# Kernel tuning notes

Hardware: AMD Instinct MI355X
Metric: run time of the kernel (lower is better)

## Reference

```python
import jax, jax.numpy as jnp
import numpy as np

B, D_IN, H, D_OUT, K = 8192, 2048, 2048, 1024, 4
LOGVAR_INIT = -5.0


def setup_inputs() -> dict:
    key = jax.random.key(0)
    ks = jax.random.split(key, 32)
    dims = [(D_IN, H), (H, H), (H, D_OUT)]
    inp = {"x": jax.random.normal(ks[0], (B, D_IN), dtype=jnp.float32)}
    i = 1
    for l, (din, dout) in enumerate(dims):
        inp[f"w_mu{l}"] = 0.1 * jax.random.normal(ks[i], (K, dout, din), dtype=jnp.float32); i += 1
        inp[f"b_mu{l}"] = 0.1 * jax.random.normal(ks[i], (K, dout), dtype=jnp.float32); i += 1
        inp[f"w_lv{l}"] = jnp.full((K,), LOGVAR_INIT, dtype=jnp.float32)
        inp[f"b_lv{l}"] = jnp.full((K,), LOGVAR_INIT, dtype=jnp.float32)
        inp[f"ml{l}"] = jnp.zeros((K,), dtype=jnp.float32)
        # reparameterization noise (randn_like in the torch code), one per component
        inp[f"w_n{l}"] = jax.random.normal(ks[i], (K, dout, din), dtype=jnp.float32); i += 1
        inp[f"b_n{l}"] = jax.random.normal(ks[i], (K, dout), dtype=jnp.float32); i += 1
    return inp


def _mixture_linear(x, w_mu, b_mu, w_lv, b_lv, ml, w_n, b_n):
    # n_components <= n_samples: all K components used, weighted by softmax(mix_logits)
    mix_w = jax.nn.softmax(ml)                               # [K]
    w = w_mu + jnp.exp(0.5 * w_lv)[:, None, None] * w_n      # [K, O, I]
    b = b_mu + jnp.exp(0.5 * b_lv)[:, None] * b_n            # [K, O]
    # sum_k mix_w[k] * (x @ w[k].T + b[k])
    out = jnp.einsum('bi,koi,k->bo', x, w, mix_w)
    out = out + jnp.einsum('k,ko->o', mix_w, b)
    return out


def reference(x,
              w_mu0, b_mu0, w_lv0, b_lv0, ml0, w_n0, b_n0,
              w_mu1, b_mu1, w_lv1, b_lv1, ml1, w_n1, b_n1,
              w_mu2, b_mu2, w_lv2, b_lv2, ml2, w_n2, b_n2):
    h = jax.nn.relu(_mixture_linear(x, w_mu0, b_mu0, w_lv0, b_lv0, ml0, w_n0, b_n0))
    h = jax.nn.relu(_mixture_linear(h, w_mu1, b_mu1, w_lv1, b_lv1, ml1, w_n1, b_n1))
    h = _mixture_linear(h, w_mu2, b_mu2, w_lv2, b_lv2, ml2, w_n2, b_n2)
    return jax.nn.softmax(h, axis=1)
```

## Files before the change

kernel.cpp:

```cpp
#include <hip/hip_runtime.h>
#include <hip/hip_fp16.h>

typedef _Float16 half8 __attribute__((ext_vector_type(8)));
typedef _Float16 half4 __attribute__((ext_vector_type(4)));
typedef float floatx16 __attribute__((ext_vector_type(16)));

#define GLDS16(g, l)                                                           \
  __builtin_amdgcn_global_load_lds(                                            \
      (const __attribute__((address_space(1))) void*)(g),                      \
      (__attribute__((address_space(3))) void*)(l), 16, 0, 0)

__device__ inline void mix_coeffs(const float* lv, const float* ml,
                                  float* cmu, float* cn) {
  float m0 = ml[0], m1 = ml[1], m2 = ml[2], m3 = ml[3];
  float mx = fmaxf(fmaxf(m0, m1), fmaxf(m2, m3));
  float e0 = __expf(m0 - mx), e1 = __expf(m1 - mx);
  float e2 = __expf(m2 - mx), e3 = __expf(m3 - mx);
  float inv = 1.0f / (e0 + e1 + e2 + e3);
  cmu[0] = e0 * inv; cmu[1] = e1 * inv; cmu[2] = e2 * inv; cmu[3] = e3 * inv;
  cn[0] = cmu[0] * __expf(0.5f * lv[0]);
  cn[1] = cmu[1] * __expf(0.5f * lv[1]);
  cn[2] = cmu[2] * __expf(0.5f * lv[2]);
  cn[3] = cmu[3] * __expf(0.5f * lv[3]);
}

__device__ inline void do_prep_w(const float* __restrict__ mu,
                                 const float* __restrict__ nz,
                                 const float* lv, const float* ml,
                                 _Float16* __restrict__ out, long count4,
                                 int bid) {
  float cmu[4], cn[4];
  mix_coeffs(lv, ml, cmu, cn);
  long i = (long)bid * 256 + threadIdx.x;
  const float4* m4 = (const float4*)mu;
  const float4* n4 = (const float4*)nz;
  float4 a0 = m4[0 * count4 + i];
  float4 a1 = m4[1 * count4 + i];
  float4 a2 = m4[2 * count4 + i];
  float4 a3 = m4[3 * count4 + i];
  float4 b0 = n4[0 * count4 + i];
  float4 b1 = n4[1 * count4 + i];
  float4 b2 = n4[2 * count4 + i];
  float4 b3 = n4[3 * count4 + i];
  float rx = cmu[0]*a0.x + cn[0]*b0.x + cmu[1]*a1.x + cn[1]*b1.x
           + cmu[2]*a2.x + cn[2]*b2.x + cmu[3]*a3.x + cn[3]*b3.x;
  float ry = cmu[0]*a0.y + cn[0]*b0.y + cmu[1]*a1.y + cn[1]*b1.y
           + cmu[2]*a2.y + cn[2]*b2.y + cmu[3]*a3.y + cn[3]*b3.y;
  float rz = cmu[0]*a0.z + cn[0]*b0.z + cmu[1]*a1.z + cn[1]*b1.z
           + cmu[2]*a2.z + cn[2]*b2.z + cmu[3]*a3.z + cn[3]*b3.z;
  float rw = cmu[0]*a0.w + cn[0]*b0.w + cmu[1]*a1.w + cn[1]*b1.w
           + cmu[2]*a2.w + cn[2]*b2.w + cmu[3]*a3.w + cn[3]*b3.w;
  half4 h = {(_Float16)rx, (_Float16)ry, (_Float16)rz, (_Float16)rw};
  *(half4*)(out + i * 4) = h;
}

__device__ inline void do_prep_b(const float* __restrict__ bmu,
                                 const float* __restrict__ bn,
                                 const float* lv, const float* ml,
                                 float* __restrict__ out, int O, int bid) {
  float cmu[4], cn[4];
  mix_coeffs(lv, ml, cmu, cn);
  int i = bid * 256 + threadIdx.x;
  if (i >= O) return;
  float r = 0.f;
#pragma unroll
  for (int k = 0; k < 4; ++k)
    r += cmu[k] * bmu[k * O + i] + cn[k] * bn[k * O + i];
  out[i] = r;
}

__device__ inline void do_cvt(const float* __restrict__ in,
                              _Float16* __restrict__ out, int bid) {
  long i = ((long)bid * 256 + threadIdx.x) * 4;
  float4 v = *(const float4*)(in + i);
  half4 h = {(_Float16)v.x, (_Float16)v.y, (_Float16)v.z, (_Float16)v.w};
  *(half4*)(out + i) = h;
}

struct PrepArgs {
  const float* x; _Float16* x16;
  const float* wmu0; const float* wn0; const float* wlv0; const float* ml0; _Float16* W0;
  const float* wmu1; const float* wn1; const float* wlv1; const float* ml1; _Float16* W1;
  const float* wmu2; const float* wn2; const float* wlv2; const float* ml2; _Float16* W2;
  const float* bmu0; const float* bn0; const float* blv0; float* b0;
  const float* bmu1; const float* bn1; const float* blv1; float* b1;
  const float* bmu2; const float* bn2; const float* blv2; float* b2;
};

__global__ __launch_bounds__(256) void prep_all(PrepArgs a) {
  for (int wb = blockIdx.x; wb < 26644; wb += 2048) {
    if (wb < 4096) {
      do_prep_w(a.wmu0, a.wn0, a.wlv0, a.ml0, a.W0, 1048576, wb);
    } else if (wb < 8192) {
      do_prep_w(a.wmu1, a.wn1, a.wlv1, a.ml1, a.W1, 1048576, wb - 4096);
    } else if (wb < 10240) {
      do_prep_w(a.wmu2, a.wn2, a.wlv2, a.ml2, a.W2, 524288, wb - 8192);
    } else if (wb < 26624) {
      do_cvt(a.x, a.x16, wb - 10240);
    } else if (wb < 26632) {
      do_prep_b(a.bmu0, a.bn0, a.blv0, a.ml0, a.b0, 2048, wb - 26624);
    } else if (wb < 26640) {
      do_prep_b(a.bmu1, a.bn1, a.blv1, a.ml1, a.b1, 2048, wb - 26632);
    } else {
      do_prep_b(a.bmu2, a.bn2, a.blv2, a.ml2, a.b2, 1024, wb - 26640);
    }
  }
}

template <bool RELU, bool OUT_HALF>
__global__ __launch_bounds__(256, 3) void gemm_nt(
    const _Float16* __restrict__ A, const _Float16* __restrict__ B,
    const float* __restrict__ bias, void* __restrict__ Cout,
    int M, int N, int K) {
  __shared__ _Float16 sA[128 * 64];
  __shared__ _Float16 sB[128 * 64];

  const int t = threadIdx.x;
  const int l = t & 63;
  const int w = t >> 6;
  const int wr = w >> 1;
  const int wc = w & 1;
  const long rowBlock = (long)blockIdx.y * 128;
  const long colBlock = (long)blockIdx.x * 128;

  floatx16 acc[2][2] = {};

  const _Float16* ga[4];
  const _Float16* gb[4];
#pragma unroll
  for (int j = 0; j < 4; ++j) {
    int p = j * 256 + t;
    int r = p >> 3, pos = p & 7;
    int gc = pos ^ (r & 7);
    ga[j] = A + (rowBlock + r) * (long)K + gc * 8;
    gb[j] = B + (colBlock + r) * (long)K + gc * 8;
  }
  char* stA = (char*)sA + w * 1024;
  char* stB = (char*)sB + w * 1024;

  const int rm = l & 31;
  const int kh = l >> 5;
  const int sw = rm & 7;

  for (int k0 = 0; k0 < K; k0 += 64) {
#pragma unroll
    for (int j = 0; j < 4; ++j) GLDS16(ga[j] + k0, stA + j * 4096);
#pragma unroll
    for (int j = 0; j < 4; ++j) GLDS16(gb[j] + k0, stB + j * 4096);
    __syncthreads();
#pragma unroll
    for (int s = 0; s < 4; ++s) {
      const int pos = (s * 2 + kh) ^ sw;
      half8 af[2], bf[2];
#pragma unroll
      for (int rt = 0; rt < 2; ++rt)
        af[rt] = *(const half8*)((const char*)sA +
                                 ((wr * 64 + rt * 32 + rm) * 128 + pos * 16));
#pragma unroll
      for (int ct = 0; ct < 2; ++ct)
        bf[ct] = *(const half8*)((const char*)sB +
                                 ((wc * 64 + ct * 32 + rm) * 128 + pos * 16));
#pragma unroll
      for (int rt = 0; rt < 2; ++rt)
#pragma unroll
        for (int ct = 0; ct < 2; ++ct)
          acc[rt][ct] = __builtin_amdgcn_mfma_f32_32x32x16_f16(
              af[rt], bf[ct], acc[rt][ct], 0, 0, 0);
    }
    __syncthreads();
  }

  const int cl = l & 31;
  const int rh = (l >> 5) * 4;
#pragma unroll
  for (int rt = 0; rt < 2; ++rt) {
#pragma unroll
    for (int ct = 0; ct < 2; ++ct) {
      const long colg = colBlock + wc * 64 + ct * 32 + cl;
      const float bv = bias[colg];
#pragma unroll
      for (int reg = 0; reg < 16; ++reg) {
        const int rowin = (reg & 3) + 8 * (reg >> 2) + rh;
        const long rowg = rowBlock + wr * 64 + rt * 32 + rowin;
        float v = acc[rt][ct][reg] + bv;
        if (RELU) v = fmaxf(v, 0.0f);
        if (OUT_HALF)
          ((_Float16*)Cout)[rowg * N + colg] = (_Float16)v;
        else
          ((float*)Cout)[rowg * N + colg] = v;
      }
    }
  }
}

__global__ __launch_bounds__(256) void softmax_rows(float* __restrict__ io) {
  const int N = 1024;
  float* p = io + (long)blockIdx.x * N;
  int t = threadIdx.x;
  int w = t >> 6;
  float4 v = ((const float4*)p)[t];
  float m = fmaxf(fmaxf(v.x, v.y), fmaxf(v.z, v.w));
#pragma unroll
  for (int off = 32; off > 0; off >>= 1) m = fmaxf(m, __shfl_xor(m, off));
  __shared__ float red[8];
  if ((t & 63) == 0) red[w] = m;
  __syncthreads();
  m = fmaxf(fmaxf(red[0], red[1]), fmaxf(red[2], red[3]));
  float4 e;
  e.x = __expf(v.x - m); e.y = __expf(v.y - m);
  e.z = __expf(v.z - m); e.w = __expf(v.w - m);
  float s = e.x + e.y + e.z + e.w;
#pragma unroll
  for (int off = 32; off > 0; off >>= 1) s += __shfl_xor(s, off);
  if ((t & 63) == 0) red[4 + w] = s;
  __syncthreads();
  s = red[4] + red[5] + red[6] + red[7];
  float inv = 1.0f / s;
  float4 o = {e.x * inv, e.y * inv, e.z * inv, e.w * inv};
  ((float4*)p)[t] = o;
}

extern "C" void kernel_launch(void* const* d_in, const int* in_sizes, int n_in,
                              void* d_out, int out_size, void* d_ws,
                              size_t ws_size, hipStream_t stream) {
  char* ws = (char*)d_ws;
  _Float16* x16 = (_Float16*)(ws);
  _Float16* h0  = (_Float16*)(ws + 33554432);
  _Float16* W0  = (_Float16*)(ws + 67108864);
  _Float16* W1  = (_Float16*)(ws + 75497472);
  _Float16* W2  = (_Float16*)(ws + 83886080);
  float* b0 = (float*)(ws + 88080384);
  float* b1 = (float*)(ws + 88088576);
  float* b2 = (float*)(ws + 88096768);

  PrepArgs a;
  a.x = (const float*)d_in[0]; a.x16 = x16;
  a.wmu0 = (const float*)d_in[1];  a.bmu0 = (const float*)d_in[2];
  a.wlv0 = (const float*)d_in[3];  a.blv0 = (const float*)d_in[4];
  a.ml0  = (const float*)d_in[5];
  a.wn0  = (const float*)d_in[6];  a.bn0  = (const float*)d_in[7];
  a.wmu1 = (const float*)d_in[8];  a.bmu1 = (const float*)d_in[9];
  a.wlv1 = (const float*)d_in[10]; a.blv1 = (const float*)d_in[11];
  a.ml1  = (const float*)d_in[12];
  a.wn1  = (const float*)d_in[13]; a.bn1  = (const float*)d_in[14];
  a.wmu2 = (const float*)d_in[15]; a.bmu2 = (const float*)d_in[16];
  a.wlv2 = (const float*)d_in[17]; a.blv2 = (const float*)d_in[18];
  a.ml2  = (const float*)d_in[19];
  a.wn2  = (const float*)d_in[20]; a.bn2  = (const float*)d_in[21];
  a.W0 = W0; a.W1 = W1; a.W2 = W2; a.b0 = b0; a.b1 = b1; a.b2 = b2;

  prep_all<<<2048, 256, 0, stream>>>(a);

  gemm_nt<true, true><<<dim3(16, 64), 256, 0, stream>>>(
      x16, W0, b0, h0, 8192, 2048, 2048);
  gemm_nt<true, true><<<dim3(16, 64), 256, 0, stream>>>(
      h0, W1, b1, x16, 8192, 2048, 2048);
  gemm_nt<false, false><<<dim3(8, 64), 256, 0, stream>>>(
      x16, W2, b2, d_out, 8192, 1024, 2048);
  softmax_rows<<<8192, 256, 0, stream>>>((float*)d_out);
}
```

Before: 617.8 us.

## Double-buffer GEMM LDS tiles, swizzle block order, and widen prep work per thread

The GEMM now uses two LDS buffers per operand and issues the global-to-LDS loads for the next K-slice before computing the current one, removing one barrier per iteration and overlapping load latency with MFMA work. Work-group ids are remapped with an XCD-style swizzle onto a 1D grid to improve L2 locality. Occupancy is lowered to 2 blocks per CU because LDS use doubles. The prep kernel also processes four float4 chunks per thread with a flat grid instead of a grid-stride loop.

```diff
diff --git a/kernel.cpp b/kernel.cpp
--- a/kernel.cpp
+++ b/kernel.cpp
@@ -24,34 +24,51 @@
   cn[3] = cmu[3] * __expf(0.5f * lv[3]);
 }
 
-__device__ inline void do_prep_w(const float* __restrict__ mu,
-                                 const float* __restrict__ nz,
-                                 const float* lv, const float* ml,
-                                 _Float16* __restrict__ out, long count4,
-                                 int bid) {
+__device__ inline void fma4(float4& acc, float cm, const float4& a, float cc,
+                            const float4& b) {
+  acc.x += cm * a.x + cc * b.x;
+  acc.y += cm * a.y + cc * b.y;
+  acc.z += cm * a.z + cc * b.z;
+  acc.w += cm * a.w + cc * b.w;
+}
+
+__device__ inline void do_prep_w4(const float* __restrict__ mu,
+                                  const float* __restrict__ nz,
+                                  const float* lv, const float* ml,
+                                  _Float16* __restrict__ out, long count4,
+                                  int bid) {
   float cmu[4], cn[4];
   mix_coeffs(lv, ml, cmu, cn);
-  long i = (long)bid * 256 + threadIdx.x;
+  long base = (long)bid * 1024 + threadIdx.x;
   const float4* m4 = (const float4*)mu;
   const float4* n4 = (const float4*)nz;
-  float4 a0 = m4[0 * count4 + i];
-  float4 a1 = m4[1 * count4 + i];
-  float4 a2 = m4[2 * count4 + i];
-  float4 a3 = m4[3 * count4 + i];
-  float4 b0 = n4[0 * count4 + i];
-  float4 b1 = n4[1 * count4 + i];
-  float4 b2 = n4[2 * count4 + i];
-  float4 b3 = n4[3 * count4 + i];
-  float rx = cmu[0]*a0.x + cn[0]*b0.x + cmu[1]*a1.x + cn[1]*b1.x
-           + cmu[2]*a2.x + cn[2]*b2.x + cmu[3]*a3.x + cn[3]*b3.x;
-  float ry = cmu[0]*a0.y + cn[0]*b0.y + cmu[1]*a1.y + cn[1]*b1.y
-           + cmu[2]*a2.y + cn[2]*b2.y + cmu[3]*a3.y + cn[3]*b3.y;
-  float rz = cmu[0]*a0.z + cn[0]*b0.z + cmu[1]*a1.z + cn[1]*b1.z
-           + cmu[2]*a2.z + cn[2]*b2.z + cmu[3]*a3.z + cn[3]*b3.z;
-  float rw = cmu[0]*a0.w + cn[0]*b0.w + cmu[1]*a1.w + cn[1]*b1.w
-           + cmu[2]*a2.w + cn[2]*b2.w + cmu[3]*a3.w + cn[3]*b3.w;
-  half4 h = {(_Float16)rx, (_Float16)ry, (_Float16)rz, (_Float16)rw};
-  *(half4*)(out + i * 4) = h;
+  float4 acc0 = {0, 0, 0, 0}, acc1 = {0, 0, 0, 0};
+  float4 acc2 = {0, 0, 0, 0}, acc3 = {0, 0, 0, 0};
+#pragma unroll
+  for (int k = 0; k < 4; ++k) {
+    long o = (long)k * count4 + base;
+    float4 a0 = m4[o];
+    float4 a1 = m4[o + 256];
+    float4 a2 = m4[o + 512];
+    float4 a3 = m4[o + 768];
+    float4 b0 = n4[o];
+    float4 b1 = n4[o + 256];
+    float4 b2 = n4[o + 512];
+    float4 b3 = n4[o + 768];
+    float cm = cmu[k], cc = cn[k];
+    fma4(acc0, cm, a0, cc, b0);
+    fma4(acc1, cm, a1, cc, b1);
+    fma4(acc2, cm, a2, cc, b2);
+    fma4(acc3, cm, a3, cc, b3);
+  }
+  half4 h0 = {(_Float16)acc0.x, (_Float16)acc0.y, (_Float16)acc0.z, (_Float16)acc0.w};
+  half4 h1 = {(_Float16)acc1.x, (_Float16)acc1.y, (_Float16)acc1.z, (_Float16)acc1.w};
+  half4 h2 = {(_Float16)acc2.x, (_Float16)acc2.y, (_Float16)acc2.z, (_Float16)acc2.w};
+  half4 h3 = {(_Float16)acc3.x, (_Float16)acc3.y, (_Float16)acc3.z, (_Float16)acc3.w};
+  *(half4*)(out + base * 4) = h0;
+  *(half4*)(out + (base + 256) * 4) = h1;
+  *(half4*)(out + (base + 512) * 4) = h2;
+  *(half4*)(out + (base + 768) * 4) = h3;
 }
 
 __device__ inline void do_prep_b(const float* __restrict__ bmu,
@@ -69,12 +86,22 @@
   out[i] = r;
 }
 
-__device__ inline void do_cvt(const float* __restrict__ in,
-                              _Float16* __restrict__ out, int bid) {
-  long i = ((long)bid * 256 + threadIdx.x) * 4;
-  float4 v = *(const float4*)(in + i);
-  half4 h = {(_Float16)v.x, (_Float16)v.y, (_Float16)v.z, (_Float16)v.w};
-  *(half4*)(out + i) = h;
+__device__ inline void do_cvt4(const float* __restrict__ in,
+                               _Float16* __restrict__ out, int bid) {
+  long base = (long)bid * 1024 + threadIdx.x;
+  const float4* in4 = (const float4*)in;
+  float4 v0 = in4[base];
+  float4 v1 = in4[base + 256];
+  float4 v2 = in4[base + 512];
+  float4 v3 = in4[base + 768];
+  half4 h0 = {(_Float16)v0.x, (_Float16)v0.y, (_Float16)v0.z, (_Float16)v0.w};
+  half4 h1 = {(_Float16)v1.x, (_Float16)v1.y, (_Float16)v1.z, (_Float16)v1.w};
+  half4 h2 = {(_Float16)v2.x, (_Float16)v2.y, (_Float16)v2.z, (_Float16)v2.w};
+  half4 h3 = {(_Float16)v3.x, (_Float16)v3.y, (_Float16)v3.z, (_Float16)v3.w};
+  *(half4*)(out + base * 4) = h0;
+  *(half4*)(out + (base + 256) * 4) = h1;
+  *(half4*)(out + (base + 512) * 4) = h2;
+  *(half4*)(out + (base + 768) * 4) = h3;
 }
 
 struct PrepArgs {
@@ -88,40 +115,43 @@
 };
 
 __global__ __launch_bounds__(256) void prep_all(PrepArgs a) {
-  for (int wb = blockIdx.x; wb < 26644; wb += 2048) {
-    if (wb < 4096) {
-      do_prep_w(a.wmu0, a.wn0, a.wlv0, a.ml0, a.W0, 1048576, wb);
-    } else if (wb < 8192) {
-      do_prep_w(a.wmu1, a.wn1, a.wlv1, a.ml1, a.W1, 1048576, wb - 4096);
-    } else if (wb < 10240) {
-      do_prep_w(a.wmu2, a.wn2, a.wlv2, a.ml2, a.W2, 524288, wb - 8192);
-    } else if (wb < 26624) {
-      do_cvt(a.x, a.x16, wb - 10240);
-    } else if (wb < 26632) {
-      do_prep_b(a.bmu0, a.bn0, a.blv0, a.ml0, a.b0, 2048, wb - 26624);
-    } else if (wb < 26640) {
-      do_prep_b(a.bmu1, a.bn1, a.blv1, a.ml1, a.b1, 2048, wb - 26632);
-    } else {
-      do_prep_b(a.bmu2, a.bn2, a.blv2, a.ml2, a.b2, 1024, wb - 26640);
-    }
-  }
+  int b = blockIdx.x;
+  if (b < 1024) { do_prep_w4(a.wmu0, a.wn0, a.wlv0, a.ml0, a.W0, 1048576, b); return; }
+  b -= 1024;
+  if (b < 1024) { do_prep_w4(a.wmu1, a.wn1, a.wlv1, a.ml1, a.W1, 1048576, b); return; }
+  b -= 1024;
+  if (b < 512) { do_prep_w4(a.wmu2, a.wn2, a.wlv2, a.ml2, a.W2, 524288, b); return; }
+  b -= 512;
+  if (b < 4096) { do_cvt4(a.x, a.x16, b); return; }
+  b -= 4096;
+  if (b < 8) { do_prep_b(a.bmu0, a.bn0, a.blv0, a.ml0, a.b0, 2048, b); return; }
+  b -= 8;
+  if (b < 8) { do_prep_b(a.bmu1, a.bn1, a.blv1, a.ml1, a.b1, 2048, b); return; }
+  b -= 8;
+  do_prep_b(a.bmu2, a.bn2, a.blv2, a.ml2, a.b2, 1024, b);
 }
 
 template <bool RELU, bool OUT_HALF>
-__global__ __launch_bounds__(256, 3) void gemm_nt(
+__global__ __launch_bounds__(256, 2) void gemm2ph(
     const _Float16* __restrict__ A, const _Float16* __restrict__ B,
     const float* __restrict__ bias, void* __restrict__ Cout,
-    int M, int N, int K) {
-  __shared__ _Float16 sA[128 * 64];
-  __shared__ _Float16 sB[128 * 64];
+    int M, int N, int K, int nbx) {
+  __shared__ _Float16 sA[2][128 * 64];
+  __shared__ _Float16 sB[2][128 * 64];
+
+  const int nwg = gridDim.x;
+  const int q = nwg >> 3;
+  const int swz = (blockIdx.x & 7) * q + (blockIdx.x >> 3);
+  const int bx = swz % nbx;
+  const int by = swz / nbx;
 
   const int t = threadIdx.x;
   const int l = t & 63;
   const int w = t >> 6;
   const int wr = w >> 1;
   const int wc = w & 1;
-  const long rowBlock = (long)blockIdx.y * 128;
-  const long colBlock = (long)blockIdx.x * 128;
+  const long rowBlock = (long)by * 128;
+  const long colBlock = (long)bx * 128;
 
   floatx16 acc[2][2] = {};
 
@@ -135,30 +165,39 @@
     ga[j] = A + (rowBlock + r) * (long)K + gc * 8;
     gb[j] = B + (colBlock + r) * (long)K + gc * 8;
   }
-  char* stA = (char*)sA + w * 1024;
-  char* stB = (char*)sB + w * 1024;
 
   const int rm = l & 31;
   const int kh = l >> 5;
   const int sw = rm & 7;
 
+#pragma unroll
+  for (int j = 0; j < 4; ++j) {
+    GLDS16(ga[j], (char*)sA[0] + w * 1024 + j * 4096);
+    GLDS16(gb[j], (char*)sB[0] + w * 1024 + j * 4096);
+  }
+  __syncthreads();
+
+  int cur = 0;
   for (int k0 = 0; k0 < K; k0 += 64) {
-#pragma unroll
-    for (int j = 0; j < 4; ++j) GLDS16(ga[j] + k0, stA + j * 4096);
-#pragma unroll
-    for (int j = 0; j < 4; ++j) GLDS16(gb[j] + k0, stB + j * 4096);
-    __syncthreads();
+    if (k0 + 64 < K) {
+      const int nxt = cur ^ 1;
+#pragma unroll
+      for (int j = 0; j < 4; ++j) {
+        GLDS16(ga[j] + k0 + 64, (char*)sA[nxt] + w * 1024 + j * 4096);
+        GLDS16(gb[j] + k0 + 64, (char*)sB[nxt] + w * 1024 + j * 4096);
+      }
+    }
 #pragma unroll
     for (int s = 0; s < 4; ++s) {
       const int pos = (s * 2 + kh) ^ sw;
       half8 af[2], bf[2];
 #pragma unroll
       for (int rt = 0; rt < 2; ++rt)
-        af[rt] = *(const half8*)((const char*)sA +
+        af[rt] = *(const half8*)((const char*)sA[cur] +
                                  ((wr * 64 + rt * 32 + rm) * 128 + pos * 16));
 #pragma unroll
       for (int ct = 0; ct < 2; ++ct)
-        bf[ct] = *(const half8*)((const char*)sB +
+        bf[ct] = *(const half8*)((const char*)sB[cur] +
                                  ((wc * 64 + ct * 32 + rm) * 128 + pos * 16));
 #pragma unroll
       for (int rt = 0; rt < 2; ++rt)
@@ -168,6 +207,7 @@
               af[rt], bf[ct], acc[rt][ct], 0, 0, 0);
     }
     __syncthreads();
+    cur ^= 1;
   }
 
   const int cl = l & 31;
@@ -249,13 +289,13 @@
   a.wn2  = (const float*)d_in[20]; a.bn2  = (const float*)d_in[21];
   a.W0 = W0; a.W1 = W1; a.W2 = W2; a.b0 = b0; a.b1 = b1; a.b2 = b2;
 
-  prep_all<<<2048, 256, 0, stream>>>(a);
-
-  gemm_nt<true, true><<<dim3(16, 64), 256, 0, stream>>>(
-      x16, W0, b0, h0, 8192, 2048, 2048);
-  gemm_nt<true, true><<<dim3(16, 64), 256, 0, stream>>>(
-      h0, W1, b1, x16, 8192, 2048, 2048);
-  gemm_nt<false, false><<<dim3(8, 64), 256, 0, stream>>>(
-      x16, W2, b2, d_out, 8192, 1024, 2048);
+  prep_all<<<6676, 256, 0, stream>>>(a);
+
+  gemm2ph<true, true><<<1024, 256, 0, stream>>>(
+      x16, W0, b0, h0, 8192, 2048, 2048, 16);
+  gemm2ph<true, true><<<1024, 256, 0, stream>>>(
+      h0, W1, b1, x16, 8192, 2048, 2048, 16);
+  gemm2ph<false, false><<<512, 256, 0, stream>>>(
+      x16, W2, b2, d_out, 8192, 1024, 2048, 8);
   softmax_rows<<<8192, 256, 0, stream>>>((float*)d_out);
 }
```

New measurement: 612.6 us. Within noise of the previous version (-0.8%).
